# Performance work log

Measured on AMD Instinct MI355X. Metric: run time of the kernel, lower is better.

Reference implementation:

```python
import jax, jax.numpy as jnp
import numpy as np

VOC, DIM = 50000, 128
B, CTX, K = 256, 8, 10


def setup_inputs() -> dict:
    key = jax.random.key(0)
    k1, k2, k3, k4, k5 = jax.random.split(key, 5)
    # one-hot inputs, as the module's math assumes (one-hot matmul == gather)
    vo_idx = jax.random.randint(k1, (B,), 0, VOC)
    vi_idx = jax.random.randint(k2, (B, CTX), 0, VOC)
    neg_idx = jax.random.randint(k3, (B, K), 0, VOC)
    vo = jax.nn.one_hot(vo_idx, VOC, dtype=jnp.float32)            # [B, VOC]
    vi = jax.nn.one_hot(vi_idx, VOC, dtype=jnp.float32)           # [B, CTX, VOC]
    neg_samples = jax.nn.one_hot(neg_idx, VOC, dtype=jnp.float32) # [B, K, VOC]
    V = jax.random.normal(k4, (VOC, DIM), dtype=jnp.float32)
    U = jax.random.normal(k5, (VOC, DIM), dtype=jnp.float32)
    return {"vo": vo, "vi": vi, "neg_samples": neg_samples, "V": V, "U": U}


def reference(vo, vi, neg_samples, V, U):
    vo_embed = vo @ V                                           # [B, D]
    # matmul(vi, U).mean(dim=1): fold mean into a single contraction
    vi_embed = jnp.einsum('bcv,vd->bd', vi, U) / vi.shape[1]    # [B, D]
    left = jax.nn.log_sigmoid(jnp.sum(vo_embed * vi_embed, axis=1, keepdims=True))  # [B,1]
    neg_embed = jnp.einsum('bkv,vd->bkd', neg_samples, U)       # [B, K, D]
    batch_mul = jnp.einsum('bkd,bd->bk', neg_embed, vo_embed)   # [B, K]
    right = jnp.sum(jax.nn.log_sigmoid(-batch_mul), axis=1, keepdims=True)          # [B,1]
    return jnp.mean(-(left + right))
```

## Files before the change

### kernel.cpp

```cpp
#include <hip/hip_runtime.h>
#include <hip/hip_bf16.h>
#include <math.h>

#define VOC 50000
#define DIM 128
#define B   256
#define CTX 8
#define K   10

#define NVEC (VOC / 4)
#define N_VO  (B)
#define N_VI  (B * CTX)
#define N_NEG (B * K)
#define NROW  (N_VO + N_VI + N_NEG)

__global__ __launch_bounds__(256) void find_indices(
    const float* __restrict__ vo,
    const float* __restrict__ vi,
    const float* __restrict__ neg,
    int* __restrict__ out_idx)
{
    const int r = blockIdx.x;
    const float* row;
    if (r < N_VO)              row = vo  + (size_t)r * VOC;
    else if (r < N_VO + N_VI)  row = vi  + (size_t)(r - N_VO) * VOC;
    else                       row = neg + (size_t)(r - N_VO - N_VI) * VOC;

    const float4* row4 = (const float4*)row;

    __shared__ int found;
    if (threadIdx.x == 0) found = -1;
    __syncthreads();

    for (int start = 0; start < NVEC; start += 256 * 4) {
#pragma unroll
        for (int j = 0; j < 4; ++j) {
            const int p = start + j * 256 + (int)threadIdx.x;
            if (p < NVEC) {
                const float4 v = row4[p];
                if (v.x != 0.f || v.y != 0.f || v.z != 0.f || v.w != 0.f) {
                    int lane_off = (v.x != 0.f) ? 0 : (v.y != 0.f) ? 1
                                 : (v.z != 0.f) ? 2 : 3;
                    found = 4 * p + lane_off;
                }
            }
        }
        __syncthreads();
        if (found >= 0) break;
    }

    if (threadIdx.x == 0) out_idx[r] = found;
}

__device__ __forceinline__ float wave_sum(float v) {
#pragma unroll
    for (int o = 32; o > 0; o >>= 1) v += __shfl_down(v, o);
    return v;
}

__device__ __forceinline__ float log_sigmoid(float x) {
    return fminf(x, 0.f) - log1pf(expf(-fabsf(x)));
}

__global__ __launch_bounds__(64) void cbow_loss(
    const float* __restrict__ V,
    const float* __restrict__ U,
    const int* __restrict__ idx_all,
    float* __restrict__ out)
{
    const int b = blockIdx.x;
    const int t = threadIdx.x;

    const int* idx_vo  = idx_all;
    const int* idx_vi  = idx_all + N_VO;
    const int* idx_neg = idx_all + N_VO + N_VI;

    const int vo_i = max(idx_vo[b], 0);
    const float v0 = V[(size_t)vo_i * DIM + t];
    const float v1 = V[(size_t)vo_i * DIM + t + 64];

    float e0 = 0.f, e1 = 0.f;
#pragma unroll
    for (int c = 0; c < CTX; ++c) {
        const int u = max(idx_vi[b * CTX + c], 0);
        e0 += U[(size_t)u * DIM + t];
        e1 += U[(size_t)u * DIM + t + 64];
    }
    e0 *= (1.f / CTX);
    e1 *= (1.f / CTX);

    const float dot_pos = wave_sum(v0 * e0 + v1 * e1);

    float right = 0.f;
#pragma unroll
    for (int k = 0; k < K; ++k) {
        const int u = max(idx_neg[b * K + k], 0);
        const float s = wave_sum(v0 * U[(size_t)u * DIM + t] +
                                 v1 * U[(size_t)u * DIM + t + 64]);
        if (t == 0) right += log_sigmoid(-s);
    }

    if (t == 0) {
        const float left = log_sigmoid(dot_pos);
        atomicAdd(out, -(left + right) * (1.f / B));
    }
}

extern "C" void kernel_launch(void* const* d_in, const int* in_sizes, int n_in,
                              void* d_out, int out_size, void* d_ws, size_t ws_size,
                              hipStream_t stream) {
    const float* vo  = (const float*)d_in[0];
    const float* vi  = (const float*)d_in[1];
    const float* neg = (const float*)d_in[2];
    const float* V   = (const float*)d_in[3];
    const float* U   = (const float*)d_in[4];
    float* out = (float*)d_out;

    int* idx_ws = (int*)d_ws;

    hipMemsetAsync(out, 0, sizeof(float), stream);

    find_indices<<<NROW, 256, 0, stream>>>(vo, vi, neg, idx_ws);
    cbow_loss<<<B, 64, 0, stream>>>(V, U, idx_ws, out);
}
```

Baseline: 866.6 us.

## Scan one-hot rows per wavefront with ballot early-exit and register prefetch

The index search now gives each 64-lane wavefront its own one-hot row, four rows per block. It replaces the block-wide shared flag and __syncthreads with a wave ballot for early exit. Each wave double-buffers float4 loads in registers so the next chunk is in flight while the current one is tested. Each wave stops at its own hit instead of waiting on a block barrier, though a row whose hot element sits late still needs a long serial scan by a single wave.

```diff
diff --git a/kernel.cpp b/kernel.cpp
--- a/kernel.cpp
+++ b/kernel.cpp
@@ -14,42 +14,86 @@
 #define N_NEG (B * K)
 #define NROW  (N_VO + N_VI + N_NEG)
 
+#define FULL_CHUNKS 48
+
+__device__ __forceinline__ bool any_nz(const float4& v) {
+    return (v.x != 0.f) | (v.y != 0.f) | (v.z != 0.f) | (v.w != 0.f);
+}
+
 __global__ __launch_bounds__(256) void find_indices(
     const float* __restrict__ vo,
     const float* __restrict__ vi,
     const float* __restrict__ neg,
     int* __restrict__ out_idx)
 {
-    const int r = blockIdx.x;
+    const int wave = blockIdx.x * 4 + ((int)threadIdx.x >> 6);
+    const int lane = (int)threadIdx.x & 63;
+
     const float* row;
-    if (r < N_VO)              row = vo  + (size_t)r * VOC;
-    else if (r < N_VO + N_VI)  row = vi  + (size_t)(r - N_VO) * VOC;
-    else                       row = neg + (size_t)(r - N_VO - N_VI) * VOC;
-
+    {
+        const int r = wave;
+        if (r < N_VO)              row = vo  + (size_t)r * VOC;
+        else if (r < N_VO + N_VI)  row = vi  + (size_t)(r - N_VO) * VOC;
+        else                       row = neg + (size_t)(r - N_VO - N_VI) * VOC;
+    }
     const float4* row4 = (const float4*)row;
 
-    __shared__ int found;
-    if (threadIdx.x == 0) found = -1;
-    __syncthreads();
+    float4 cur[4];
+#pragma unroll
+    for (int j = 0; j < 4; ++j) cur[j] = row4[j * 64 + lane];
 
-    for (int start = 0; start < NVEC; start += 256 * 4) {
+    int base = 0;
+    for (int c = 0; c < FULL_CHUNKS; ++c) {
+        float4 nxt[4];
+        const int nb = base + 256;
+        if (c + 1 < FULL_CHUNKS) {
+#pragma unroll
+            for (int j = 0; j < 4; ++j) nxt[j] = row4[nb + j * 64 + lane];
+        } else {
+#pragma unroll
+            for (int j = 0; j < 4; ++j) {
+                const int p = nb + j * 64 + lane;
+                nxt[j] = (p < NVEC) ? row4[p] : make_float4(0.f, 0.f, 0.f, 0.f);
+            }
+        }
+
+        const bool pred = any_nz(cur[0]) | any_nz(cur[1]) |
+                          any_nz(cur[2]) | any_nz(cur[3]);
+        const unsigned long long m = __ballot(pred);
+        if (m) {
+            if (pred) {
+                int idx = -1;
+#pragma unroll
+                for (int j = 0; j < 4; ++j) {
+                    const int p = base + j * 64 + lane;
+                    if (cur[j].x != 0.f) idx = 4 * p;
+                    if (cur[j].y != 0.f) idx = 4 * p + 1;
+                    if (cur[j].z != 0.f) idx = 4 * p + 2;
+                    if (cur[j].w != 0.f) idx = 4 * p + 3;
+                }
+                out_idx[wave] = idx;
+            }
+            return;
+        }
+#pragma unroll
+        for (int j = 0; j < 4; ++j) cur[j] = nxt[j];
+        base = nb;
+    }
+
+    const bool pred = any_nz(cur[0]) | any_nz(cur[1]) |
+                      any_nz(cur[2]) | any_nz(cur[3]);
+    if (pred) {
+        int idx = -1;
 #pragma unroll
         for (int j = 0; j < 4; ++j) {
-            const int p = start + j * 256 + (int)threadIdx.x;
-            if (p < NVEC) {
-                const float4 v = row4[p];
-                if (v.x != 0.f || v.y != 0.f || v.z != 0.f || v.w != 0.f) {
-                    int lane_off = (v.x != 0.f) ? 0 : (v.y != 0.f) ? 1
-                                 : (v.z != 0.f) ? 2 : 3;
-                    found = 4 * p + lane_off;
-                }
-            }
+            const int p = base + j * 64 + lane;
+            if (cur[j].x != 0.f) idx = 4 * p;
+            if (cur[j].y != 0.f) idx = 4 * p + 1;
+            if (cur[j].z != 0.f) idx = 4 * p + 2;
+            if (cur[j].w != 0.f) idx = 4 * p + 3;
         }
-        __syncthreads();
-        if (found >= 0) break;
+        out_idx[wave] = idx;
     }
-
-    if (threadIdx.x == 0) out_idx[r] = found;
 }
 
 __device__ __forceinline__ float wave_sum(float v) {
@@ -120,6 +164,6 @@
 
     hipMemsetAsync(out, 0, sizeof(float), stream);
 
-    find_indices<<<NROW, 256, 0, stream>>>(vo, vi, neg, idx_ws);
+    find_indices<<<NROW / 4, 256, 0, stream>>>(vo, vi, neg, idx_ws);
     cbow_loss<<<B, 64, 0, stream>>>(V, U, idx_ws, out);
 }
```

Result: no change. 878.0 us (+1.3%).
